# Optimization experiments

Hardware: AMD Instinct MI355X
Metric: run time of the kernel (lower is better)

Reference implementation:

```python
import jax, jax.numpy as jnp
import numpy as np

BLOCK = 8
ITERS = 8
EPS = 1e-5
SHAPE = (64, 64, 64)
BATCH = 16


def overlapping_blocks(x, bs):
    # x: [B, M, N, K] -> per-block copies with a 1-cell zero-padded halo:
    # [B, nm, nn, nk, bs+2, bs+2, bs+2]
    B, M, N, K = x.shape
    p = jnp.pad(x, ((0, 0), (1, 1), (1, 1), (1, 1)))

    def gather(a, axis, n, size):
        idx = (jnp.arange(n)[:, None] * bs + jnp.arange(size)[None, :]).reshape(-1)
        a = jnp.take(a, idx, axis=axis)
        return a.reshape(a.shape[:axis] + (n, size) + a.shape[axis + 1:])

    nm, nn, nk = M // bs, N // bs, K // bs
    p = gather(p, 1, nm, bs + 2)   # [B, nm, P, N+2, K+2]
    p = gather(p, 3, nn, bs + 2)   # [B, nm, P, nn, P, K+2]
    p = gather(p, 5, nk, bs + 2)   # [B, nm, P, nn, P, nk, P]
    return p.transpose(0, 1, 3, 5, 2, 4, 6)


def param_blocks(w, bs):
    # [..., M, N, K] -> [..., nm, nn, nk, bs, bs, bs] (non-overlapping)
    lead = w.shape[:-3]
    M, N, K = w.shape[-3:]
    w = w.reshape(*lead, M // bs, bs, N // bs, bs, K // bs, bs)
    nl = len(lead)
    perm = tuple(range(nl)) + (nl, nl + 2, nl + 4, nl + 1, nl + 3, nl + 5)
    return w.transpose(perm)


def gridnet_step(weight, bias, residual_scale, x, inner_iterations, block_size,
                 eps=EPS, normalize=True):
    bs = block_size
    blocks = overlapping_blocks(x, bs)            # [B, nm, nn, nk, P, P, P]
    wb = param_blocks(weight, bs)                 # [27, nm, nn, nk, bs, bs, bs]
    bb = param_blocks(bias, bs)                   # [nm, nn, nk, bs, bs, bs]
    rb = param_blocks(residual_scale, bs)
    inner = (slice(None),) * 4 + (slice(1, -1),) * 3

    for _ in range(inner_iterations):
        if normalize:
            mean = blocks.mean(axis=(-3, -2, -1), keepdims=True)
            var = blocks.var(axis=(-3, -2, -1), keepdims=True)
            normed = (blocks - mean) / jnp.sqrt(var + eps)
        else:
            normed = blocks
        dot = jnp.zeros_like(blocks[inner])
        tap = 0
        for dx in range(3):
            for dy in range(3):
                for dz in range(3):
                    nb = normed[..., dx:dx + bs, dy:dy + bs, dz:dz + bs]
                    dot = dot + nb * wb[tap]
                    tap += 1
        out = blocks[inner] + rb * jax.nn.silu(dot + bb)
        # only interior cells update; halo stays at initial (synced) values
        blocks = blocks.at[inner].set(out)

    y = blocks[inner]                              # [B, nm, nn, nk, bs, bs, bs]
    B, nm, nn, nk = y.shape[:4]
    return y.transpose(0, 1, 4, 2, 5, 3, 6).reshape(B, nm * bs, nn * bs, nk * bs)


def setup_inputs() -> dict:
    key = jax.random.key(0)
    k_w, k_x = jax.random.split(key)
    M, N, K = SHAPE
    weight = jax.random.normal(k_w, (27, M, N, K), dtype=jnp.float32) / np.sqrt(27.0).astype(np.float32)
    bias = jnp.zeros((M, N, K), dtype=jnp.float32)
    residual_scale = jnp.ones((M, N, K), dtype=jnp.float32)
    x = jax.random.normal(k_x, (BATCH, M, N, K), dtype=jnp.float32)
    return {"weight": weight, "bias": bias, "residual_scale": residual_scale, "x": x}


def reference(weight, bias, residual_scale, x):
    return gridnet_step(weight, bias, residual_scale, x, ITERS, BLOCK, EPS, True)
```

## Files before the change

### kernel.cpp

```cpp
#include <hip/hip_runtime.h>

typedef _Float16 h2 __attribute__((ext_vector_type(2)));

#define COLH 10

template <int CTRL>
__device__ __forceinline__ float dpp_stage(float v) {
    int x = __builtin_amdgcn_update_dpp(0, __float_as_int(v), CTRL, 0xf, 0xf, true);
    return v + __int_as_float(x);
}
__device__ __forceinline__ float wave_sum(float v) {
    v = dpp_stage<0x111>(v);
    v = dpp_stage<0x112>(v);
    v = dpp_stage<0x114>(v);
    v = dpp_stage<0x118>(v);
    v = dpp_stage<0x142>(v);
    v = dpp_stage<0x143>(v);
    return v;
}

#define RFL(x) __int_as_float(__builtin_amdgcn_readfirstlane(__float_as_int(x)))

__device__ __forceinline__ h2 mid2(h2 lo, h2 hi) {
    int r = __builtin_amdgcn_alignbit(__builtin_bit_cast(int, hi),
                                      __builtin_bit_cast(int, lo), 16);
    return __builtin_bit_cast(h2, r);
}

#define R27(M) M(0) M(1) M(2) M(3) M(4) M(5) M(6) M(7) M(8) M(9) M(10) M(11) \
    M(12) M(13) M(14) M(15) M(16) M(17) M(18) M(19) M(20) M(21) M(22) M(23)  \
    M(24) M(25) M(26)
#define R9L(M) M(0) M(1) M(2) M(3) M(4) M(5) M(6) M(7) M(8)

#define LOADW(T) float2 f##T = *(const float2*)(W + ((size_t)(T) << 18) + ofs); \
                 h2 w##T = { (_Float16)f##T.x, (_Float16)f##T.y };              \
                 sw0 += (float)w##T.x; sw1 += (float)w##T.y;

#define LINE(L, WA, WB, WC) {                                                 \
    const h2 v0 = bp[(((L) / 3) * 10 + (L) % 3) * 5];                         \
    const h2 v1 = bp[(((L) / 3) * 10 + (L) % 3) * 5 + 1];                     \
    const h2 vm = mid2(v0, v1);                                               \
    dd = __builtin_elementwise_fma(v0, WA, dd);                               \
    dd = __builtin_elementwise_fma(vm, WB, dd);                               \
    dd = __builtin_elementwise_fma(v1, WC, dd);  }

#define ITER(SRC, DST, RED) {                                                 \
    const h2* bp = (const h2*)&SRC[base_h];                                   \
    float mean = (halo_s + Si) * inv_n;                                       \
    float istd = rsqrtf((halo_q + Qi) * inv_n - mean * mean + 1e-5f);         \
    h2 dd = { (_Float16)0.f, (_Float16)0.f };                                 \
    LINE(0, w0,  w1,  w2)                                                     \
    LINE(1, w3,  w4,  w5)                                                     \
    LINE(2, w6,  w7,  w8)                                                     \
    LINE(3, w9,  w10, w11)                                                    \
    LINE(4, w12, w13, w14)                                                    \
    LINE(5, w15, w16, w17)                                                    \
    LINE(6, w18, w19, w20)                                                    \
    LINE(7, w21, w22, w23)                                                    \
    LINE(8, w24, w25, w26)                                                    \
    float u0 = ((float)dd.x - mean * sw0) * istd + bias0;                     \
    float u1 = ((float)dd.y - mean * sw1) * istd + bias1;                     \
    c0 += rs0 * (u0 * __builtin_amdgcn_rcpf(1.f + __expf(-u0)));              \
    c1 += rs1 * (u1 * __builtin_amdgcn_rcpf(1.f + __expf(-u1)));              \
    DST[ipc]     = (_Float16)c0;                                              \
    DST[ipc + 1] = (_Float16)c1;                                              \
    float b0 = wave_sum(c0 + c1);                                             \
    float b1 = wave_sum(c0 * c0 + c1 * c1);                                   \
    if (lane == 63) RED[wave] = make_float2(b0, b1);                          \
    __syncthreads();                                                          \
    Si = RFL(RED[0].x + RED[1].x + RED[2].x + RED[3].x);                      \
    Qi = RFL(RED[0].y + RED[1].y + RED[2].y + RED[3].y); }

__global__ __launch_bounds__(256)
void gridnet_kernel(const float* __restrict__ W,
                    const float* __restrict__ Bias,
                    const float* __restrict__ Rs,
                    const float* __restrict__ X,
                    float* __restrict__ Y,
                    int n_batch)
{
    __shared__ __align__(16) _Float16 buf0[100 * COLH];
    __shared__ __align__(16) _Float16 buf1[100 * COLH];
    __shared__ float4 red4[4];
    __shared__ float2 redA[4], redB[4];

    const int tid  = threadIdx.x;
    const int h    = tid & 3;
    const int ly   = (tid >> 2) & 7;
    const int lx   = tid >> 5;
    const int wave = tid >> 6;
    const int lane = tid & 63;

    const int bid   = blockIdx.x;
    const int r     = bid / n_batch;
    const int batch = bid - r * n_batch;
    const int gm0 = (r >> 6) << 3;
    const int gn0 = ((r >> 3) & 7) << 3;
    const int gk0 = (r & 7) << 3;

    const float* xb = X + ((size_t)batch << 18);

    float s_all = 0.f, q_all = 0.f, s_int = 0.f, q_int = 0.f;
    for (int i = tid; i < 1000; i += 256) {
        int ix = i / 100;
        int rem = i - ix * 100;
        int iy = rem / 10;
        int iz = rem - iy * 10;
        int m = gm0 + ix - 1, n = gn0 + iy - 1, k = gk0 + iz - 1;
        float v = 0.f;
        if ((unsigned)m < 64u && (unsigned)n < 64u && (unsigned)k < 64u)
            v = xb[(m << 12) + (n << 6) + k];
        _Float16 hv = (_Float16)v;
        int a = (ix * 10 + iy) * COLH + iz;
        buf0[a] = hv;
        buf1[a] = hv;
        float vf = (float)hv;
        s_all += vf;
        q_all += vf * vf;
        bool interior = ((unsigned)(ix - 1) < 8u) & ((unsigned)(iy - 1) < 8u) &
                        ((unsigned)(iz - 1) < 8u);
        if (interior) { s_int += vf; q_int += vf * vf; }
    }

    const int gm = gm0 + lx, gn = gn0 + ly, gk = gk0 + 2 * h;
    const size_t ofs = ((size_t)gm << 12) + (gn << 6) + gk;

    float sw0 = 0.f, sw1 = 0.f;
    R27(LOADW)
    const float2 bf = *(const float2*)(Bias + ofs);
    const float2 rf = *(const float2*)(Rs + ofs);
    const float bias0 = bf.x, bias1 = bf.y;
    const float rs0 = rf.x, rs1 = rf.y;

    __syncthreads();

    const int base_h = (lx * 10 + ly) * COLH + 2 * h;
    const int ipc    = ((lx + 1) * 10 + (ly + 1)) * COLH + (2 * h + 1);
    float c0 = (float)buf0[ipc];
    float c1 = (float)buf0[ipc + 1];

    float a0 = wave_sum(s_all);
    float a1 = wave_sum(q_all);
    float a2 = wave_sum(s_int);
    float a3 = wave_sum(q_int);
    if (lane == 63) red4[wave] = make_float4(a0, a1, a2, a3);
    __syncthreads();
    float S_all = 0.f, Q_all = 0.f, Si = 0.f, Qi = 0.f;
    #pragma unroll
    for (int wv = 0; wv < 4; ++wv) {
        float4 t4 = red4[wv];
        S_all += t4.x; Q_all += t4.y; Si += t4.z; Qi += t4.w;
    }
    const float halo_s = RFL(S_all - Si);
    const float halo_q = RFL(Q_all - Qi);
    Si = RFL(Si);
    Qi = RFL(Qi);

    const float inv_n = 1.0f / 1000.0f;

    #pragma unroll 1
    for (int it = 0; it < 4; ++it) {
        ITER(buf0, buf1, redA)
        ITER(buf1, buf0, redB)
    }

    *(float2*)(Y + ((size_t)batch << 18) + ofs) = make_float2(c0, c1);
}

extern "C" void kernel_launch(void* const* d_in, const int* in_sizes, int n_in,
                              void* d_out, int out_size, void* d_ws, size_t ws_size,
                              hipStream_t stream) {
    const float* W = (const float*)d_in[0];
    const float* B = (const float*)d_in[1];
    const float* R = (const float*)d_in[2];
    const float* X = (const float*)d_in[3];
    float* Y = (float*)d_out;

    int n_batch = in_sizes[3] >> 18;
    dim3 grid(512 * n_batch), block(256);
    hipLaunchKernelGGL(gridnet_kernel, grid, block, 0, stream, W, B, R, X, Y, n_batch);
}
```

Measured before the change: 166.0 us.

## Shrink each block to one wave with eight z-cells per thread, dropping block barriers

Each grid block now uses a single 64-thread wave. Each thread owns a full 8-cell z-line and keeps its 27x4 packed half-precision weights in registers. Because the block is one wave, mean and variance come from wave-wide DPP reductions with a readlane broadcast, so the double LDS buffer and the per-iteration __syncthreads are gone. The stencil reuses each loaded 10-value column across four packed accumulators, halo rows are loaded as float4, and block indices are swizzled. The risks are higher register pressure from holding the weights in registers, and relying on in-wave lockstep order for the in-place LDS update.

Result: slower. 231.8 us (+39.6%).

```diff
diff --git a/kernel.cpp b/kernel.cpp
--- a/kernel.cpp
+++ b/kernel.cpp
@@ -1,8 +1,6 @@
 #include <hip/hip_runtime.h>
 
 typedef _Float16 h2 __attribute__((ext_vector_type(2)));
-
-#define COLH 10
 
 template <int CTRL>
 __device__ __forceinline__ float dpp_stage(float v) {
@@ -18,60 +16,45 @@
     v = dpp_stage<0x143>(v);
     return v;
 }
-
-#define RFL(x) __int_as_float(__builtin_amdgcn_readfirstlane(__float_as_int(x)))
-
+__device__ __forceinline__ float bcast63(float v) {
+    return __int_as_float(__builtin_amdgcn_readlane(__float_as_int(v), 63));
+}
 __device__ __forceinline__ h2 mid2(h2 lo, h2 hi) {
     int r = __builtin_amdgcn_alignbit(__builtin_bit_cast(int, hi),
                                       __builtin_bit_cast(int, lo), 16);
     return __builtin_bit_cast(h2, r);
 }
-
-#define R27(M) M(0) M(1) M(2) M(3) M(4) M(5) M(6) M(7) M(8) M(9) M(10) M(11) \
-    M(12) M(13) M(14) M(15) M(16) M(17) M(18) M(19) M(20) M(21) M(22) M(23)  \
-    M(24) M(25) M(26)
-#define R9L(M) M(0) M(1) M(2) M(3) M(4) M(5) M(6) M(7) M(8)
-
-#define LOADW(T) float2 f##T = *(const float2*)(W + ((size_t)(T) << 18) + ofs); \
-                 h2 w##T = { (_Float16)f##T.x, (_Float16)f##T.y };              \
-                 sw0 += (float)w##T.x; sw1 += (float)w##T.y;
-
-#define LINE(L, WA, WB, WC) {                                                 \
-    const h2 v0 = bp[(((L) / 3) * 10 + (L) % 3) * 5];                         \
-    const h2 v1 = bp[(((L) / 3) * 10 + (L) % 3) * 5 + 1];                     \
-    const h2 vm = mid2(v0, v1);                                               \
-    dd = __builtin_elementwise_fma(v0, WA, dd);                               \
-    dd = __builtin_elementwise_fma(vm, WB, dd);                               \
-    dd = __builtin_elementwise_fma(v1, WC, dd);  }
-
-#define ITER(SRC, DST, RED) {                                                 \
-    const h2* bp = (const h2*)&SRC[base_h];                                   \
-    float mean = (halo_s + Si) * inv_n;                                       \
-    float istd = rsqrtf((halo_q + Qi) * inv_n - mean * mean + 1e-5f);         \
-    h2 dd = { (_Float16)0.f, (_Float16)0.f };                                 \
-    LINE(0, w0,  w1,  w2)                                                     \
-    LINE(1, w3,  w4,  w5)                                                     \
-    LINE(2, w6,  w7,  w8)                                                     \
-    LINE(3, w9,  w10, w11)                                                    \
-    LINE(4, w12, w13, w14)                                                    \
-    LINE(5, w15, w16, w17)                                                    \
-    LINE(6, w18, w19, w20)                                                    \
-    LINE(7, w21, w22, w23)                                                    \
-    LINE(8, w24, w25, w26)                                                    \
-    float u0 = ((float)dd.x - mean * sw0) * istd + bias0;                     \
-    float u1 = ((float)dd.y - mean * sw1) * istd + bias1;                     \
-    c0 += rs0 * (u0 * __builtin_amdgcn_rcpf(1.f + __expf(-u0)));              \
-    c1 += rs1 * (u1 * __builtin_amdgcn_rcpf(1.f + __expf(-u1)));              \
-    DST[ipc]     = (_Float16)c0;                                              \
-    DST[ipc + 1] = (_Float16)c1;                                              \
-    float b0 = wave_sum(c0 + c1);                                             \
-    float b1 = wave_sum(c0 * c0 + c1 * c1);                                   \
-    if (lane == 63) RED[wave] = make_float2(b0, b1);                          \
-    __syncthreads();                                                          \
-    Si = RFL(RED[0].x + RED[1].x + RED[2].x + RED[3].x);                      \
-    Qi = RFL(RED[0].y + RED[1].y + RED[2].y + RED[3].y); }
-
-__global__ __launch_bounds__(256)
+__device__ __forceinline__ h2 pkrtz(float a, float b) {
+    return __builtin_bit_cast(h2, __builtin_amdgcn_cvt_pkrtz(a, b));
+}
+
+#define MEMFENCE() asm volatile("" ::: "memory")
+
+#define COL(DX, DY) {                                                          \
+    const int o = 5 * (10 * (DX) + (DY));                                      \
+    h2 D0 = bp[o + 0], D1 = bp[o + 1], D2 = bp[o + 2], D3 = bp[o + 3],         \
+       D4 = bp[o + 4];                                                         \
+    h2 M0 = mid2(D0, D1), M1 = mid2(D1, D2), M2 = mid2(D2, D3),                \
+       M3 = mid2(D3, D4);                                                      \
+    const int tA = ((DX) * 3 + (DY)) * 3;                                      \
+    dd0 = __builtin_elementwise_fma(D0, w[tA][0], dd0);                        \
+    dd1 = __builtin_elementwise_fma(D1, w[tA][1], dd1);                        \
+    dd2 = __builtin_elementwise_fma(D2, w[tA][2], dd2);                        \
+    dd3 = __builtin_elementwise_fma(D3, w[tA][3], dd3);                        \
+    dd0 = __builtin_elementwise_fma(M0, w[tA + 1][0], dd0);                    \
+    dd1 = __builtin_elementwise_fma(M1, w[tA + 1][1], dd1);                    \
+    dd2 = __builtin_elementwise_fma(M2, w[tA + 1][2], dd2);                    \
+    dd3 = __builtin_elementwise_fma(M3, w[tA + 1][3], dd3);                    \
+    dd0 = __builtin_elementwise_fma(D1, w[tA + 2][0], dd0);                    \
+    dd1 = __builtin_elementwise_fma(D2, w[tA + 2][1], dd1);                    \
+    dd2 = __builtin_elementwise_fma(D3, w[tA + 2][2], dd2);                    \
+    dd3 = __builtin_elementwise_fma(D4, w[tA + 2][3], dd3); }
+
+#define OUTK(CK, DDF, SWK, BK, RK) {                                           \
+    float u = fmaf(fmaf(SWK, nmean, DDF), istd, BK);                           \
+    CK += RK * (u * __builtin_amdgcn_rcpf(1.f + __expf(-u))); }
+
+__global__ __launch_bounds__(64)
 void gridnet_kernel(const float* __restrict__ W,
                     const float* __restrict__ Bias,
                     const float* __restrict__ Rs,
@@ -79,19 +62,16 @@
                     float* __restrict__ Y,
                     int n_batch)
 {
-    __shared__ __align__(16) _Float16 buf0[100 * COLH];
-    __shared__ __align__(16) _Float16 buf1[100 * COLH];
-    __shared__ float4 red4[4];
-    __shared__ float2 redA[4], redB[4];
-
-    const int tid  = threadIdx.x;
-    const int h    = tid & 3;
-    const int ly   = (tid >> 2) & 7;
-    const int lx   = tid >> 5;
-    const int wave = tid >> 6;
-    const int lane = tid & 63;
-
-    const int bid   = blockIdx.x;
+    __shared__ __align__(16) h2 buf[500];
+
+    const int tid = threadIdx.x;
+    const int lx  = tid >> 3;
+    const int ly  = tid & 7;
+
+    const int nwg = (int)gridDim.x;
+    const int b0  = (int)blockIdx.x;
+    const int bid = (b0 & 7) * (nwg >> 3) + (b0 >> 3);
+
     const int r     = bid / n_batch;
     const int batch = bid - r * n_batch;
     const int gm0 = (r >> 6) << 3;
@@ -101,70 +81,109 @@
     const float* xb = X + ((size_t)batch << 18);
 
     float s_all = 0.f, q_all = 0.f, s_int = 0.f, q_int = 0.f;
-    for (int i = tid; i < 1000; i += 256) {
-        int ix = i / 100;
-        int rem = i - ix * 100;
-        int iy = rem / 10;
-        int iz = rem - iy * 10;
-        int m = gm0 + ix - 1, n = gn0 + iy - 1, k = gk0 + iz - 1;
-        float v = 0.f;
-        if ((unsigned)m < 64u && (unsigned)n < 64u && (unsigned)k < 64u)
-            v = xb[(m << 12) + (n << 6) + k];
-        _Float16 hv = (_Float16)v;
-        int a = (ix * 10 + iy) * COLH + iz;
-        buf0[a] = hv;
-        buf1[a] = hv;
-        float vf = (float)hv;
-        s_all += vf;
-        q_all += vf * vf;
-        bool interior = ((unsigned)(ix - 1) < 8u) & ((unsigned)(iy - 1) < 8u) &
-                        ((unsigned)(iz - 1) < 8u);
-        if (interior) { s_int += vf; q_int += vf * vf; }
+    #pragma unroll 1
+    for (int c = tid; c < 100; c += 64) {
+        int x = c / 10, y = c - (c / 10) * 10;
+        int m = gm0 + x - 1, n = gn0 + y - 1;
+        bool row_ok = ((unsigned)m < 64u) & ((unsigned)n < 64u);
+        float4 fa = {0.f, 0.f, 0.f, 0.f}, fb = {0.f, 0.f, 0.f, 0.f};
+        float vz0 = 0.f, vz9 = 0.f;
+        if (row_ok) {
+            const float* rp = xb + (m * 4096 + n * 64);
+            fa = *(const float4*)(rp + gk0);
+            fb = *(const float4*)(rp + gk0 + 4);
+            if (gk0 > 0)  vz0 = rp[gk0 - 1];
+            if (gk0 < 56) vz9 = rp[gk0 + 8];
+        }
+        h2 d0 = pkrtz(vz0, fa.x), d1 = pkrtz(fa.y, fa.z), d2 = pkrtz(fa.w, fb.x),
+           d3 = pkrtz(fb.y, fb.z), d4 = pkrtz(fb.w, vz9);
+        buf[c * 5 + 0] = d0; buf[c * 5 + 1] = d1; buf[c * 5 + 2] = d2;
+        buf[c * 5 + 3] = d3; buf[c * 5 + 4] = d4;
+        float t0 = (float)d0.x, t1 = (float)d0.y, t2 = (float)d1.x,
+              t3 = (float)d1.y, t4 = (float)d2.x, t5 = (float)d2.y,
+              t6 = (float)d3.x, t7 = (float)d3.y, t8 = (float)d4.x,
+              t9 = (float)d4.y;
+        float s8 = t1 + t2 + t3 + t4 + t5 + t6 + t7 + t8;
+        float q8 = t1*t1 + t2*t2 + t3*t3 + t4*t4 + t5*t5 + t6*t6 + t7*t7 + t8*t8;
+        s_all += s8 + t0 + t9;
+        q_all += q8 + t0*t0 + t9*t9;
+        bool inter = ((unsigned)(x - 1) < 8u) & ((unsigned)(y - 1) < 8u);
+        if (inter) { s_int += s8; q_int += q8; }
     }
-
-    const int gm = gm0 + lx, gn = gn0 + ly, gk = gk0 + 2 * h;
-    const size_t ofs = ((size_t)gm << 12) + (gn << 6) + gk;
-
-    float sw0 = 0.f, sw1 = 0.f;
-    R27(LOADW)
-    const float2 bf = *(const float2*)(Bias + ofs);
-    const float2 rf = *(const float2*)(Rs + ofs);
-    const float bias0 = bf.x, bias1 = bf.y;
-    const float rs0 = rf.x, rs1 = rf.y;
-
-    __syncthreads();
-
-    const int base_h = (lx * 10 + ly) * COLH + 2 * h;
-    const int ipc    = ((lx + 1) * 10 + (ly + 1)) * COLH + (2 * h + 1);
-    float c0 = (float)buf0[ipc];
-    float c1 = (float)buf0[ipc + 1];
-
-    float a0 = wave_sum(s_all);
-    float a1 = wave_sum(q_all);
-    float a2 = wave_sum(s_int);
-    float a3 = wave_sum(q_int);
-    if (lane == 63) red4[wave] = make_float4(a0, a1, a2, a3);
-    __syncthreads();
-    float S_all = 0.f, Q_all = 0.f, Si = 0.f, Qi = 0.f;
+    MEMFENCE();
+
+    const int gm = gm0 + lx, gn = gn0 + ly;
+    const size_t ofs = ((size_t)gm << 12) + (gn << 6) + gk0;
+    h2 w[27][4];
+    float sw0=0.f, sw1=0.f, sw2=0.f, sw3=0.f, sw4=0.f, sw5=0.f, sw6=0.f, sw7=0.f;
     #pragma unroll
-    for (int wv = 0; wv < 4; ++wv) {
-        float4 t4 = red4[wv];
-        S_all += t4.x; Q_all += t4.y; Si += t4.z; Qi += t4.w;
+    for (int t = 0; t < 27; ++t) {
+        const float* wp = W + ((size_t)t << 18) + ofs;
+        float4 fa = *(const float4*)(wp);
+        float4 fb = *(const float4*)(wp + 4);
+        w[t][0] = pkrtz(fa.x, fa.y); w[t][1] = pkrtz(fa.z, fa.w);
+        w[t][2] = pkrtz(fb.x, fb.y); w[t][3] = pkrtz(fb.z, fb.w);
+        sw0 += fa.x; sw1 += fa.y; sw2 += fa.z; sw3 += fa.w;
+        sw4 += fb.x; sw5 += fb.y; sw6 += fb.z; sw7 += fb.w;
     }
-    const float halo_s = RFL(S_all - Si);
-    const float halo_q = RFL(Q_all - Qi);
-    Si = RFL(Si);
-    Qi = RFL(Qi);
+    float4 ba = *(const float4*)(Bias + ofs), bb = *(const float4*)(Bias + ofs + 4);
+    float4 ra = *(const float4*)(Rs + ofs),   rb = *(const float4*)(Rs + ofs + 4);
+
+    float S_all = bcast63(wave_sum(s_all));
+    float Q_all = bcast63(wave_sum(q_all));
+    float Si    = bcast63(wave_sum(s_int));
+    float Qi    = bcast63(wave_sum(q_int));
+    const float halo_s = S_all - Si;
+    const float halo_q = Q_all - Qi;
+
+    h2* bp = &buf[5 * (lx * 10 + ly)];
+    h2 e0 = bp[55], e1 = bp[56], e2 = bp[57], e3 = bp[58], e4 = bp[59];
+    float z0f = (float)e0.x, z9f = (float)e4.y;
+    float c1 = (float)e0.y, c2 = (float)e1.x, c3 = (float)e1.y, c4 = (float)e2.x,
+          c5 = (float)e2.y, c6 = (float)e3.x, c7 = (float)e3.y, c8 = (float)e4.x;
 
     const float inv_n = 1.0f / 1000.0f;
 
     #pragma unroll 1
-    for (int it = 0; it < 4; ++it) {
-        ITER(buf0, buf1, redA)
-        ITER(buf1, buf0, redB)
+    for (int it = 0; it < 8; ++it) {
+        float mean  = (halo_s + Si) * inv_n;
+        float qmean = (halo_q + Qi) * inv_n;
+        float istd  = rsqrtf(qmean - mean * mean + 1e-5f);
+        float nmean = -mean;
+
+        h2 dd0 = { (_Float16)0.f, (_Float16)0.f };
+        h2 dd1 = dd0, dd2 = dd0, dd3 = dd0;
+        COL(0,0) COL(0,1) COL(0,2)
+        COL(1,0) COL(1,1) COL(1,2)
+        COL(2,0) COL(2,1) COL(2,2)
+
+        MEMFENCE();
+
+        OUTK(c1, (float)dd0.x, sw0, ba.x, ra.x)
+        OUTK(c2, (float)dd0.y, sw1, ba.y, ra.y)
+        OUTK(c3, (float)dd1.x, sw2, ba.z, ra.z)
+        OUTK(c4, (float)dd1.y, sw3, ba.w, ra.w)
+        OUTK(c5, (float)dd2.x, sw4, bb.x, rb.x)
+        OUTK(c6, (float)dd2.y, sw5, bb.y, rb.y)
+        OUTK(c7, (float)dd3.x, sw6, bb.z, rb.z)
+        OUTK(c8, (float)dd3.y, sw7, bb.w, rb.w)
+
+        e0 = pkrtz(z0f, c1); e1 = pkrtz(c2, c3); e2 = pkrtz(c4, c5);
+        e3 = pkrtz(c6, c7); e4 = pkrtz(c8, z9f);
+        bp[55] = e0; bp[56] = e1; bp[57] = e2; bp[58] = e3; bp[59] = e4;
+
+        MEMFENCE();
+
+        float sp = ((c1 + c2) + (c3 + c4)) + ((c5 + c6) + (c7 + c8));
+        float qp = ((c1*c1 + c2*c2) + (c3*c3 + c4*c4)) +
+                   ((c5*c5 + c6*c6) + (c7*c7 + c8*c8));
+        Si = bcast63(wave_sum(sp));
+        Qi = bcast63(wave_sum(qp));
     }
 
-    *(float2*)(Y + ((size_t)batch << 18) + ofs) = make_float2(c0, c1);
+    float* yp = Y + ((size_t)batch << 18) + ofs;
+    *(float4*)(yp)     = make_float4(c1, c2, c3, c4);
+    *(float4*)(yp + 4) = make_float4(c5, c6, c7, c8);
 }
 
 extern "C" void kernel_launch(void* const* d_in, const int* in_sizes, int n_in,
@@ -177,6 +196,6 @@
     float* Y = (float*)d_out;
 
     int n_batch = in_sizes[3] >> 18;
-    dim3 grid(512 * n_batch), block(256);
+    dim3 grid(512 * n_batch), block(64);
     hipLaunchKernelGGL(gridnet_kernel, grid, block, 0, stream, W, B, R, X, Y, n_batch);
 }
```

## Process two batch elements per workgroup to share weights and halve barriers

Applied to the files above, without the earlier changes.

Each workgroup now handles a pair of batch items for the same spatial block. The 27 weight taps, bias and residual scale are loaded once and reused for both, and the per-iteration block reduction and barrier are shared by the two items. This also gives each thread two independent FMA chains to interleave. In exchange it uses twice the LDS, more registers and half as many workgroups, and it assumes an even batch size.

New measurement: 154.2 us. -7.1%, faster.

```diff
diff --git a/kernel.cpp b/kernel.cpp
--- a/kernel.cpp
+++ b/kernel.cpp
@@ -30,46 +30,60 @@
 #define R27(M) M(0) M(1) M(2) M(3) M(4) M(5) M(6) M(7) M(8) M(9) M(10) M(11) \
     M(12) M(13) M(14) M(15) M(16) M(17) M(18) M(19) M(20) M(21) M(22) M(23)  \
     M(24) M(25) M(26)
-#define R9L(M) M(0) M(1) M(2) M(3) M(4) M(5) M(6) M(7) M(8)
 
 #define LOADW(T) float2 f##T = *(const float2*)(W + ((size_t)(T) << 18) + ofs); \
                  h2 w##T = { (_Float16)f##T.x, (_Float16)f##T.y };              \
                  sw0 += (float)w##T.x; sw1 += (float)w##T.y;
 
-#define LINE(L, WA, WB, WC) {                                                 \
-    const h2 v0 = bp[(((L) / 3) * 10 + (L) % 3) * 5];                         \
-    const h2 v1 = bp[(((L) / 3) * 10 + (L) % 3) * 5 + 1];                     \
+#define LINE(BP, DD, L, WA, WB, WC) {                                         \
+    const h2 v0 = BP[(((L) / 3) * 10 + (L) % 3) * 5];                         \
+    const h2 v1 = BP[(((L) / 3) * 10 + (L) % 3) * 5 + 1];                     \
     const h2 vm = mid2(v0, v1);                                               \
-    dd = __builtin_elementwise_fma(v0, WA, dd);                               \
-    dd = __builtin_elementwise_fma(vm, WB, dd);                               \
-    dd = __builtin_elementwise_fma(v1, WC, dd);  }
-
-#define ITER(SRC, DST, RED) {                                                 \
-    const h2* bp = (const h2*)&SRC[base_h];                                   \
-    float mean = (halo_s + Si) * inv_n;                                       \
-    float istd = rsqrtf((halo_q + Qi) * inv_n - mean * mean + 1e-5f);         \
-    h2 dd = { (_Float16)0.f, (_Float16)0.f };                                 \
-    LINE(0, w0,  w1,  w2)                                                     \
-    LINE(1, w3,  w4,  w5)                                                     \
-    LINE(2, w6,  w7,  w8)                                                     \
-    LINE(3, w9,  w10, w11)                                                    \
-    LINE(4, w12, w13, w14)                                                    \
-    LINE(5, w15, w16, w17)                                                    \
-    LINE(6, w18, w19, w20)                                                    \
-    LINE(7, w21, w22, w23)                                                    \
-    LINE(8, w24, w25, w26)                                                    \
-    float u0 = ((float)dd.x - mean * sw0) * istd + bias0;                     \
-    float u1 = ((float)dd.y - mean * sw1) * istd + bias1;                     \
-    c0 += rs0 * (u0 * __builtin_amdgcn_rcpf(1.f + __expf(-u0)));              \
-    c1 += rs1 * (u1 * __builtin_amdgcn_rcpf(1.f + __expf(-u1)));              \
-    DST[ipc]     = (_Float16)c0;                                              \
-    DST[ipc + 1] = (_Float16)c1;                                              \
-    float b0 = wave_sum(c0 + c1);                                             \
-    float b1 = wave_sum(c0 * c0 + c1 * c1);                                   \
-    if (lane == 63) RED[wave] = make_float2(b0, b1);                          \
+    DD = __builtin_elementwise_fma(v0, WA, DD);                               \
+    DD = __builtin_elementwise_fma(vm, WB, DD);                               \
+    DD = __builtin_elementwise_fma(v1, WC, DD);  }
+
+#define DOT9(BP, DD)                                                          \
+    LINE(BP, DD, 0, w0,  w1,  w2)                                             \
+    LINE(BP, DD, 1, w3,  w4,  w5)                                             \
+    LINE(BP, DD, 2, w6,  w7,  w8)                                             \
+    LINE(BP, DD, 3, w9,  w10, w11)                                            \
+    LINE(BP, DD, 4, w12, w13, w14)                                            \
+    LINE(BP, DD, 5, w15, w16, w17)                                            \
+    LINE(BP, DD, 6, w18, w19, w20)                                            \
+    LINE(BP, DD, 7, w21, w22, w23)                                            \
+    LINE(BP, DD, 8, w24, w25, w26)
+
+#define EPI(SFX, DST) {                                                       \
+    float mean = (halo_s##SFX + Si##SFX) * inv_n;                             \
+    float istd = rsqrtf((halo_q##SFX + Qi##SFX) * inv_n - mean*mean + 1e-5f); \
+    float u0 = ((float)dd##SFX.x - mean * sw0) * istd + bias0;                \
+    float u1 = ((float)dd##SFX.y - mean * sw1) * istd + bias1;                \
+    c0##SFX += rs0 * (u0 * __builtin_amdgcn_rcpf(1.f + __expf(-u0)));         \
+    c1##SFX += rs1 * (u1 * __builtin_amdgcn_rcpf(1.f + __expf(-u1)));         \
+    DST[ipc]     = (_Float16)c0##SFX;                                         \
+    DST[ipc + 1] = (_Float16)c1##SFX;  }
+
+#define ITERPAIR(SA, DA, SB, DB, RED) {                                       \
+    const h2* bpA = (const h2*)&SA[base_h];                                   \
+    const h2* bpB = (const h2*)&SB[base_h];                                   \
+    h2 ddA = { (_Float16)0.f, (_Float16)0.f };                                \
+    h2 ddB = ddA;                                                             \
+    DOT9(bpA, ddA)                                                            \
+    DOT9(bpB, ddB)                                                            \
+    EPI(A, DA)                                                                \
+    EPI(B, DB)                                                                \
+    float spA = wave_sum(c0A + c1A);                                          \
+    float qpA = wave_sum(c0A * c0A + c1A * c1A);                              \
+    float spB = wave_sum(c0B + c1B);                                          \
+    float qpB = wave_sum(c0B * c0B + c1B * c1B);                              \
+    if (lane == 63) { RED[0][wave] = make_float2(spA, qpA);                   \
+                      RED[1][wave] = make_float2(spB, qpB); }                 \
     __syncthreads();                                                          \
-    Si = RFL(RED[0].x + RED[1].x + RED[2].x + RED[3].x);                      \
-    Qi = RFL(RED[0].y + RED[1].y + RED[2].y + RED[3].y); }
+    SiA = RFL(RED[0][0].x + RED[0][1].x + RED[0][2].x + RED[0][3].x);         \
+    QiA = RFL(RED[0][0].y + RED[0][1].y + RED[0][2].y + RED[0][3].y);         \
+    SiB = RFL(RED[1][0].x + RED[1][1].x + RED[1][2].x + RED[1][3].x);         \
+    QiB = RFL(RED[1][0].y + RED[1][1].y + RED[1][2].y + RED[1][3].y); }
 
 __global__ __launch_bounds__(256)
 void gridnet_kernel(const float* __restrict__ W,
@@ -79,10 +93,12 @@
                     float* __restrict__ Y,
                     int n_batch)
 {
-    __shared__ __align__(16) _Float16 buf0[100 * COLH];
-    __shared__ __align__(16) _Float16 buf1[100 * COLH];
-    __shared__ float4 red4[4];
-    __shared__ float2 redA[4], redB[4];
+    __shared__ __align__(16) _Float16 bufA0[100 * COLH];
+    __shared__ __align__(16) _Float16 bufA1[100 * COLH];
+    __shared__ __align__(16) _Float16 bufB0[100 * COLH];
+    __shared__ __align__(16) _Float16 bufB1[100 * COLH];
+    __shared__ float4 red4[8];
+    __shared__ float2 redP[2][2][4];
 
     const int tid  = threadIdx.x;
     const int h    = tid & 3;
@@ -91,35 +107,43 @@
     const int wave = tid >> 6;
     const int lane = tid & 63;
 
+    const int np    = n_batch >> 1;
     const int bid   = blockIdx.x;
-    const int r     = bid / n_batch;
-    const int batch = bid - r * n_batch;
+    const int r     = bid / np;
+    const int pb    = bid - r * np;
+    const int batch = 2 * pb;
     const int gm0 = (r >> 6) << 3;
     const int gn0 = ((r >> 3) & 7) << 3;
     const int gk0 = (r & 7) << 3;
 
-    const float* xb = X + ((size_t)batch << 18);
-
-    float s_all = 0.f, q_all = 0.f, s_int = 0.f, q_int = 0.f;
+    const float* xbA = X + ((size_t)batch << 18);
+
+    float sA_all = 0.f, qA_all = 0.f, sA_int = 0.f, qA_int = 0.f;
+    float sB_all = 0.f, qB_all = 0.f, sB_int = 0.f, qB_int = 0.f;
     for (int i = tid; i < 1000; i += 256) {
         int ix = i / 100;
         int rem = i - ix * 100;
         int iy = rem / 10;
         int iz = rem - iy * 10;
         int m = gm0 + ix - 1, n = gn0 + iy - 1, k = gk0 + iz - 1;
-        float v = 0.f;
-        if ((unsigned)m < 64u && (unsigned)n < 64u && (unsigned)k < 64u)
-            v = xb[(m << 12) + (n << 6) + k];
-        _Float16 hv = (_Float16)v;
+        float vA = 0.f, vB = 0.f;
+        if ((unsigned)m < 64u && (unsigned)n < 64u && (unsigned)k < 64u) {
+            const float* p = xbA + (m << 12) + (n << 6) + k;
+            vA = p[0];
+            vB = p[1 << 18];
+        }
+        _Float16 hvA = (_Float16)vA;
+        _Float16 hvB = (_Float16)vB;
         int a = (ix * 10 + iy) * COLH + iz;
-        buf0[a] = hv;
-        buf1[a] = hv;
-        float vf = (float)hv;
-        s_all += vf;
-        q_all += vf * vf;
+        bufA0[a] = hvA; bufA1[a] = hvA;
+        bufB0[a] = hvB; bufB1[a] = hvB;
+        float fA = (float)hvA, fB = (float)hvB;
+        sA_all += fA; qA_all += fA * fA;
+        sB_all += fB; qB_all += fB * fB;
         bool interior = ((unsigned)(ix - 1) < 8u) & ((unsigned)(iy - 1) < 8u) &
                         ((unsigned)(iz - 1) < 8u);
-        if (interior) { s_int += vf; q_int += vf * vf; }
+        if (interior) { sA_int += fA; qA_int += fA * fA;
+                        sB_int += fB; qB_int += fB * fB; }
     }
 
     const int gm = gm0 + lx, gn = gn0 + ly, gk = gk0 + 2 * h;
@@ -136,35 +160,53 @@
 
     const int base_h = (lx * 10 + ly) * COLH + 2 * h;
     const int ipc    = ((lx + 1) * 10 + (ly + 1)) * COLH + (2 * h + 1);
-    float c0 = (float)buf0[ipc];
-    float c1 = (float)buf0[ipc + 1];
-
-    float a0 = wave_sum(s_all);
-    float a1 = wave_sum(q_all);
-    float a2 = wave_sum(s_int);
-    float a3 = wave_sum(q_int);
-    if (lane == 63) red4[wave] = make_float4(a0, a1, a2, a3);
+    float c0A = (float)bufA0[ipc];
+    float c1A = (float)bufA0[ipc + 1];
+    float c0B = (float)bufB0[ipc];
+    float c1B = (float)bufB0[ipc + 1];
+
+    {
+        float a0 = wave_sum(sA_all);
+        float a1 = wave_sum(qA_all);
+        float a2 = wave_sum(sA_int);
+        float a3 = wave_sum(qA_int);
+        float b0 = wave_sum(sB_all);
+        float b1 = wave_sum(qB_all);
+        float b2 = wave_sum(sB_int);
+        float b3 = wave_sum(qB_int);
+        if (lane == 63) {
+            red4[wave]     = make_float4(a0, a1, a2, a3);
+            red4[4 + wave] = make_float4(b0, b1, b2, b3);
+        }
+    }
     __syncthreads();
-    float S_all = 0.f, Q_all = 0.f, Si = 0.f, Qi = 0.f;
+    float SA_all = 0.f, QA_all = 0.f, SiA = 0.f, QiA = 0.f;
+    float SB_all = 0.f, QB_all = 0.f, SiB = 0.f, QiB = 0.f;
     #pragma unroll
     for (int wv = 0; wv < 4; ++wv) {
-        float4 t4 = red4[wv];
-        S_all += t4.x; Q_all += t4.y; Si += t4.z; Qi += t4.w;
-    }
-    const float halo_s = RFL(S_all - Si);
-    const float halo_q = RFL(Q_all - Qi);
-    Si = RFL(Si);
-    Qi = RFL(Qi);
+        float4 tA = red4[wv];
+        float4 tB = red4[4 + wv];
+        SA_all += tA.x; QA_all += tA.y; SiA += tA.z; QiA += tA.w;
+        SB_all += tB.x; QB_all += tB.y; SiB += tB.z; QiB += tB.w;
+    }
+    const float halo_sA = RFL(SA_all - SiA);
+    const float halo_qA = RFL(QA_all - QiA);
+    const float halo_sB = RFL(SB_all - SiB);
+    const float halo_qB = RFL(QB_all - QiB);
+    SiA = RFL(SiA); QiA = RFL(QiA);
+    SiB = RFL(SiB); QiB = RFL(QiB);
 
     const float inv_n = 1.0f / 1000.0f;
 
     #pragma unroll 1
     for (int it = 0; it < 4; ++it) {
-        ITER(buf0, buf1, redA)
-        ITER(buf1, buf0, redB)
-    }
-
-    *(float2*)(Y + ((size_t)batch << 18) + ofs) = make_float2(c0, c1);
+        ITERPAIR(bufA0, bufA1, bufB0, bufB1, redP[0])
+        ITERPAIR(bufA1, bufA0, bufB1, bufB0, redP[1])
+    }
+
+    float* yp = Y + ((size_t)batch << 18) + ofs;
+    *(float2*)(yp)             = make_float2(c0A, c1A);
+    *(float2*)(yp + (1 << 18)) = make_float2(c0B, c1B);
 }
 
 extern "C" void kernel_launch(void* const* d_in, const int* in_sizes, int n_in,
@@ -177,6 +219,6 @@
     float* Y = (float*)d_out;
 
     int n_batch = in_sizes[3] >> 18;
-    dim3 grid(512 * n_batch), block(256);
+    dim3 grid(512 * (n_batch >> 1)), block(256);
     hipLaunchKernelGGL(gridnet_kernel, grid, block, 0, stream, W, B, R, X, Y, n_batch);
 }
```
